# Kernel tuning notes

Hardware: AMD Instinct MI355X
Metric: run time of the kernel (lower is better)

The kernel has to match this reference:

```python
import jax, jax.numpy as jnp
import numpy as np
from math import factorial, comb

N_NODES = 50000
N_EDGES = 640000
FEAT = 32
NUM_BASIS = 8
CUTOFF = 5.0
MAX_Z = 118
NUM_ITERS = 3
LMAX = 2
K = (LMAX + 1) ** 2  # 9 spherical channels for max_degree=2


def _assoc_legendre(c, s, lmax):
    # associated Legendre P_l^m without Condon-Shortley phase
    P = {(0, 0): np.ones_like(c)}
    for m in range(1, lmax + 1):
        P[(m, m)] = P[(m - 1, m - 1)] * (2 * m - 1) * s
    for m in range(lmax):
        P[(m + 1, m)] = (2 * m + 1) * c * P[(m, m)]
    for m in range(lmax + 1):
        for l in range(m + 2, lmax + 1):
            P[(l, m)] = ((2 * l - 1) * c * P[(l - 1, m)] - (l + m - 1) * P[(l - 2, m)]) / (l - m)
    return P


def _real_sh_np(xyz, lmax):
    # Racah-normalized real spherical harmonics (Y_00 = 1), order m=-l..l
    r = np.linalg.norm(xyz, axis=1)
    cth = xyz[:, 2] / r
    sth = np.sqrt(np.maximum(1.0 - cth ** 2, 0.0))
    phi = np.arctan2(xyz[:, 1], xyz[:, 0])
    P = _assoc_legendre(cth, sth, lmax)
    cols = []
    for l in range(lmax + 1):
        for m in range(-l, l + 1):
            am = abs(m)
            if m == 0:
                cols.append(P[(l, 0)])
            else:
                nrm = np.sqrt(2.0 * factorial(l - am) / factorial(l + am))
                ang = np.cos(am * phi) if m > 0 else np.sin(am * phi)
                cols.append(nrm * P[(l, am)] * ang)
    return np.stack(cols, axis=1)


def _gaunt_tensor():
    # cg[k1,k2,k3]: expansion of Y_k1 * Y_k2 onto Y_k3 (degrees <= 2).
    # Products of degree<=2 harmonics lie exactly in span of degree<=4 harmonics,
    # so the least-squares fit below recovers exact coefficients.
    rng = np.random.default_rng(0)
    pts = rng.normal(size=(4096, 3))
    pts /= np.linalg.norm(pts, axis=1, keepdims=True)
    A = _real_sh_np(pts, 2 * LMAX)  # (M, 25)
    Y = A[:, :K]                    # (M, 9)
    prod = (Y[:, :, None] * Y[:, None, :]).reshape(len(pts), K * K)
    coef, *_ = np.linalg.lstsq(A, prod, rcond=None)  # (25, 81)
    return coef[:K].reshape(K, K, K).transpose(1, 2, 0).astype(np.float32)


CG = jnp.asarray(_gaunt_tensor())  # (9, 9, 9)
LOG_BINOM = jnp.asarray([np.log(comb(NUM_BASIS - 1, kk)) for kk in range(NUM_BASIS)], dtype=jnp.float32)


def _sh_l2(u):
    # Racah real SH of unit vectors, degrees 0..2, order m=-l..l
    x, y, z = u[:, 0], u[:, 1], u[:, 2]
    s3 = 1.7320508075688772
    return jnp.stack([
        jnp.ones_like(x),
        y, z, x,
        s3 * x * y, s3 * y * z, 0.5 * (3.0 * z * z - 1.0), s3 * x * z, 0.5 * s3 * (x * x - y * y),
    ], axis=1)


def _radial(r):
    # reciprocal Bernstein basis (log-space, stable) * smooth cutoff
    u = r / (1.0 + r)
    k = jnp.arange(NUM_BASIS, dtype=jnp.float32)
    n = float(NUM_BASIS - 1)
    eps = 1e-12
    logu = jnp.log(jnp.maximum(u, eps))[:, None]
    log1u = jnp.log(jnp.maximum(1.0 - u, eps))[:, None]
    bern = jnp.exp(LOG_BINOM + k * logu + (n - k) * log1u)  # (E, B)
    cut = jnp.where(r < CUTOFF, jnp.exp(-(r * r) / jnp.maximum(CUTOFF * CUTOFF - r * r, eps)), 0.0)
    return bern * cut[:, None]


def _forward(dr_vec, embed, rad_w, d1w, d1b, d2w, d2b, Z, neighbor_idxs):
    idx_i, idx_j = neighbor_idxs[0], neighbor_idxs[1]
    r = jnp.linalg.norm(dr_vec, axis=1)
    u = dr_vec / jnp.maximum(r, 1e-9)[:, None]
    Ysh = _sh_l2(u)              # (E, 9) angular basis
    rad = _radial(r)             # (E, B) radial basis
    # mask padding edges (idx_i == idx_j) as in mask_by_neighbor
    rad = rad * (idx_i != idx_j).astype(rad.dtype)[:, None]

    N = Z.shape[0]
    x = jnp.zeros((N, K, FEAT), jnp.float32).at[:, 0, :].set(embed[Z])

    for i in range(NUM_ITERS):
        last = i == NUM_ITERS - 1
        k3 = 1 if last else K    # last MessagePass has max_degree=0
        xe = x[idx_j]                                  # (E, 9, F) edge gather
        g = jnp.einsum('eb,dbf->edf', rad, rad_w[i])   # (E, 3, F) radial->feature per basis degree
        y = jnp.zeros((N_EDGES, k3, FEAT), jnp.float32)
        for l2 in range(LMAX + 1):
            sl = slice(l2 * l2, (l2 + 1) ** 2)
            c = jnp.einsum('abc,eb->eac', CG[:, sl, :k3], Ysh[:, sl])          # (E, 9, k3)
            y = y + jnp.einsum('eac,eaf->ecf', c, xe * g[:, l2][:, None, :])   # (E, k3, F)
        m = jax.ops.segment_sum(y, idx_i, num_segments=N)                      # scatter-sum
        if last:
            x = x[:, :1, :]      # change_max_degree_or_type(x, 0)
        h = x + m
        h = jnp.einsum('nkf,fg->nkg', h, d1w[i]).at[:, 0, :].add(d1b[i])
        gate = jax.nn.sigmoid(h[:, :1, :])
        h = h * gate             # silu on scalar channel, sigmoid-gated tensor channels
        h = jnp.einsum('nkf,fg->nkg', h, d2w[i]).at[:, 0, :].add(d2b[i])
        x = x + h
    return x[:, 0, :]            # (N, F)


def setup_inputs() -> dict:
    key = jax.random.key(0)
    ks = jax.random.split(key, 8)
    dr_vec = jax.random.normal(ks[0], (N_EDGES, 3), jnp.float32) * 2.0
    Z = jax.random.randint(ks[1], (N_NODES,), 0, MAX_Z + 1, jnp.int32)
    neighbor_idxs = jax.random.randint(ks[2], (2, N_EDGES), 0, N_NODES, jnp.int32)
    embed = jax.random.normal(ks[3], (MAX_Z + 1, FEAT), jnp.float32)
    rad_w = jax.random.normal(ks[4], (NUM_ITERS, LMAX + 1, NUM_BASIS, FEAT), jnp.float32) * 0.5
    d1w = jax.random.normal(ks[5], (NUM_ITERS, FEAT, FEAT), jnp.float32) * (1.0 / np.sqrt(FEAT))
    d1b = jnp.zeros((NUM_ITERS, FEAT), jnp.float32)
    d2w = jax.random.normal(ks[6], (NUM_ITERS, FEAT, FEAT), jnp.float32) * 0.02
    d2b = jnp.zeros((NUM_ITERS, FEAT), jnp.float32)
    return {"dr_vec": dr_vec, "embed": embed, "rad_w": rad_w, "d1w": d1w, "d1b": d1b,
            "d2w": d2w, "d2b": d2b, "Z": Z, "neighbor_idxs": neighbor_idxs}


def reference(dr_vec, embed, rad_w, d1w, d1b, d2w, d2b, Z, neighbor_idxs):
    return _forward(dr_vec, embed, rad_w, d1w, d1b, d2w, d2b, Z, neighbor_idxs)
```

## Files before the change

kernel.cpp:

```cpp
#include <hip/hip_runtime.h>
#include <hip/hip_fp16.h>
#include <math.h>

#define NN 50000
#define NE 640000
#define F  32
#define KCH 9
#define CUT 5.0f

#define C13 (1.0f/3.0f)
#define C23 (2.0f/3.0f)
#define C15 0.2f
#define C25 0.4f
#define C17 (1.0f/7.0f)
#define C27 (2.0f/7.0f)
#define IS3 0.5773502691896258f
#define S35 0.3464101615137755f
#define S37 0.2474358296526968f
#define S3  1.7320508075688772f

#define XH_NODE_B 768

union U2H { unsigned int u; __half2 h; };

__device__ __forceinline__ unsigned int pack2(float a, float b) {
    U2H c; c.h = __floats2half2_rn(a, b); return c.u;
}
__device__ __forceinline__ float2 unpack2(unsigned int u) {
    U2H c; c.u = u; return __half22float2(c.h);
}

__global__ __launch_bounds__(256) void init_x(const float* __restrict__ embed,
                                              const int* __restrict__ Z,
                                              float* __restrict__ x,
                                              char* __restrict__ xh) {
    int idx = blockIdx.x * 256 + threadIdx.x;
    int n = idx >> 5, f = idx & 31;
    float v = embed[Z[n] * F + f];
    float* xp = x + (size_t)n * KCH * F + f;
    xp[0] = v;
    #pragma unroll
    for (int a = 1; a < KCH; ++a) xp[a * F] = 0.f;
    char* bp = xh + (size_t)n * XH_NODE_B + f * 24;
    uint2 u0; u0.x = pack2(v, 0.f); u0.y = 0u;
    uint2 zz; zz.x = 0u; zz.y = 0u;
    *(uint2*)bp = u0;
    *(uint2*)(bp + 8) = zz;
    *(uint2*)(bp + 16) = zz;
}

__global__ __launch_bounds__(256) void hist_kernel(const int* __restrict__ idx_i,
                                                   const int* __restrict__ idx_j,
                                                   const float* __restrict__ dr,
                                                   int* __restrict__ cnt) {
    int e = blockIdx.x * 256 + threadIdx.x;
    if (e >= NE) return;
    int ni = idx_i[e], nj = idx_j[e];
    float dx = dr[3 * e + 0], dy = dr[3 * e + 1], dz = dr[3 * e + 2];
    float r2 = fmaf(dx, dx, fmaf(dy, dy, dz * dz));
    if (ni != nj && r2 < CUT * CUT) atomicAdd(&cnt[ni], 1);
}

#define SCAN_T 1024
#define SCAN_C ((NN + SCAN_T - 1) / SCAN_T)

__global__ __launch_bounds__(SCAN_T) void scan_kernel(const int* __restrict__ cnt,
                                                      int* __restrict__ offs,
                                                      int* __restrict__ head) {
    __shared__ int ps[SCAN_T];
    int t = threadIdx.x;
    int b = t * SCAN_C;
    int e = min(b + SCAN_C, NN);
    int s = 0;
    for (int i = b; i < e; ++i) s += cnt[i];
    ps[t] = s;
    __syncthreads();
    for (int off = 1; off < SCAN_T; off <<= 1) {
        int v = (t >= off) ? ps[t - off] : 0;
        __syncthreads();
        ps[t] += v;
        __syncthreads();
    }
    int run = (t == 0) ? 0 : ps[t - 1];
    for (int i = b; i < e; ++i) { int c = cnt[i]; offs[i] = run; head[i] = run; run += c; }
    if (t == SCAN_T - 1) offs[NN] = ps[SCAN_T - 1];
}

__global__ __launch_bounds__(256) void fill_kernel(const int* __restrict__ idx_i,
                                                   const int* __restrict__ idx_j,
                                                   const float* __restrict__ dr,
                                                   int* __restrict__ head,
                                                   float4* __restrict__ geo) {
    int e = blockIdx.x * 256 + threadIdx.x;
    if (e >= NE) return;
    int ni = idx_i[e], nj = idx_j[e];
    float dx = dr[3 * e + 0], dy = dr[3 * e + 1], dz = dr[3 * e + 2];
    float r2 = fmaf(dx, dx, fmaf(dy, dy, dz * dz));
    if (!(ni != nj && r2 < CUT * CUT)) return;

    float r = sqrtf(r2);
    float inv = 1.0f / fmaxf(r, 1e-9f);
    float ux = dx * inv, uy = dy * inv, uz = dz * inv;

    float cut = expf(-r2 / fmaxf(CUT * CUT - r2, 1e-12f));
    float ur = r / (1.0f + r), vr = 1.0f - ur;
    float up2 = ur*ur, up3 = up2*ur, up4 = up3*ur, up5 = up4*ur, up6 = up5*ur, up7 = up6*ur;
    float vp2 = vr*vr, vp3 = vp2*vr, vp4 = vp3*vr, vp5 = vp4*vr, vp6 = vp5*vr, vp7 = vp6*vr;

    int p = atomicAdd(&head[ni], 1);
    float4 gA, gB, gC;
    gA.x = ux; gA.y = uy; gA.z = uz; gA.w = __int_as_float(nj);
    gB.x = cut * vp7;
    gB.y = cut * 7.f  * ur  * vp6;
    gB.z = cut * 21.f * up2 * vp5;
    gB.w = cut * 35.f * up3 * vp4;
    gC.x = cut * 35.f * up4 * vp3;
    gC.y = cut * 21.f * up5 * vp2;
    gC.z = cut * 7.f  * up6 * vr;
    gC.w = cut * up7;
    geo[(size_t)3 * p + 0] = gA;
    geo[(size_t)3 * p + 1] = gB;
    geo[(size_t)3 * p + 2] = gC;
}

template<int LAST>
__global__ __launch_bounds__(256) void gather_kernel(const float4* __restrict__ geo,
                                                     const char* __restrict__ xh,
                                                     const float* __restrict__ rw_iter,
                                                     const int* __restrict__ offs,
                                                     float* __restrict__ m) {
    const int NWAVES = 2048 * 4;
    int lane = threadIdx.x & 63;
    int wid  = threadIdx.x >> 6;
    int half = lane >> 5;
    int f    = lane & 31;
    int gw   = blockIdx.x * 4 + wid;

    float rwv[24];
    #pragma unroll
    for (int lb = 0; lb < 24; ++lb) rwv[lb] = rw_iter[lb * F + f];
    if (LAST) {
        #pragma unroll
        for (int lb = 8; lb < 16; ++lb) rwv[lb] *= C13;
        #pragma unroll
        for (int lb = 16; lb < 24; ++lb) rwv[lb] *= C15;
    }

    constexpr int NACC = LAST ? 1 : KCH;

    for (int n = gw; n < NN; n += NWAVES) {
        int start = offs[n], end = offs[n + 1];

        float acc[NACC];
        #pragma unroll
        for (int a = 0; a < NACC; ++a) acc[a] = 0.f;

        int t = start + half;
        float4 gA_c = {}, gB_c = {}, gC_c = {}, gA_n = {};
        uint2 xa = {}, xb = {};
        unsigned int xc = 0;

        if (t < end) {
            gA_c = geo[(size_t)3 * t + 0];
            gB_c = geo[(size_t)3 * t + 1];
            gC_c = geo[(size_t)3 * t + 2];
            int njc = __float_as_int(gA_c.w);
            const char* bp = xh + (size_t)njc * XH_NODE_B + f * 24;
            xa = *(const uint2*)bp;
            xb = *(const uint2*)(bp + 8);
            xc = *(const unsigned int*)(bp + 16);
            int t2 = (t + 2 < end) ? t + 2 : t;
            gA_n = geo[(size_t)3 * t2 + 0];
        }

        while (t < end) {
            int tn = t + 2;
            int tnc = (tn < end) ? tn : t;
            int tfc = (tn + 2 < end) ? tn + 2 : tnc;

            float4 gA_f = geo[(size_t)3 * tfc + 0];
            float4 gB_n = geo[(size_t)3 * tnc + 1];
            float4 gC_n = geo[(size_t)3 * tnc + 2];
            int njn = __float_as_int(gA_n.w);
            const char* bp = xh + (size_t)njn * XH_NODE_B + f * 24;
            uint2 na = *(const uint2*)bp;
            uint2 nb = *(const uint2*)(bp + 8);
            unsigned int nc = *(const unsigned int*)(bp + 16);

            float xe[9];
            {
                float2 p;
                p = unpack2(xa.x); xe[0] = p.x; xe[1] = p.y;
                p = unpack2(xa.y); xe[2] = p.x; xe[3] = p.y;
                p = unpack2(xb.x); xe[4] = p.x; xe[5] = p.y;
                p = unpack2(xb.y); xe[6] = p.x; xe[7] = p.y;
                p = unpack2(xc);   xe[8] = p.x;
            }

            float ux = gA_c.x, uy = gA_c.y, uz = gA_c.z;
            float g0, g1, g2;
            g0 = gB_c.x * rwv[0];
            g0 = fmaf(gB_c.y, rwv[1], g0); g0 = fmaf(gB_c.z, rwv[2], g0); g0 = fmaf(gB_c.w, rwv[3], g0);
            g0 = fmaf(gC_c.x, rwv[4], g0); g0 = fmaf(gC_c.y, rwv[5], g0); g0 = fmaf(gC_c.z, rwv[6], g0);
            g0 = fmaf(gC_c.w, rwv[7], g0);
            g1 = gB_c.x * rwv[8];
            g1 = fmaf(gB_c.y, rwv[9],  g1); g1 = fmaf(gB_c.z, rwv[10], g1); g1 = fmaf(gB_c.w, rwv[11], g1);
            g1 = fmaf(gC_c.x, rwv[12], g1); g1 = fmaf(gC_c.y, rwv[13], g1); g1 = fmaf(gC_c.z, rwv[14], g1);
            g1 = fmaf(gC_c.w, rwv[15], g1);
            g2 = gB_c.x * rwv[16];
            g2 = fmaf(gB_c.y, rwv[17], g2); g2 = fmaf(gB_c.z, rwv[18], g2); g2 = fmaf(gB_c.w, rwv[19], g2);
            g2 = fmaf(gC_c.x, rwv[20], g2); g2 = fmaf(gC_c.y, rwv[21], g2); g2 = fmaf(gC_c.z, rwv[22], g2);
            g2 = fmaf(gC_c.w, rwv[23], g2);

            if (LAST) {
                float dot1 = uy * xe[1];
                dot1 = fmaf(uz, xe[2], dot1);
                dot1 = fmaf(ux, xe[3], dot1);
                float Y4 = S3 * ux * uy, Y5 = S3 * uy * uz, Y7 = S3 * ux * uz;
                float Y6 = fmaf(1.5f * uz, uz, -0.5f);
                float Y8 = 0.5f * S3 * (ux * ux - uy * uy);
                float dot2 = Y4 * xe[4];
                dot2 = fmaf(Y5, xe[5], dot2);
                dot2 = fmaf(Y6, xe[6], dot2);
                dot2 = fmaf(Y7, xe[7], dot2);
                dot2 = fmaf(Y8, xe[8], dot2);
                acc[0] = fmaf(g0, xe[0], acc[0]);
                acc[0] = fmaf(g1, dot1, acc[0]);
                acc[0] = fmaf(g2, dot2, acc[0]);
            } else {
                float s2 = S3 * g2;
                float w[9];
                w[0] = g0;
                w[1] = uy * g1; w[2] = uz * g1; w[3] = ux * g1;
                w[4] = s2 * ux * uy;
                w[5] = s2 * uy * uz;
                w[6] = fmaf(1.5f * uz, uz, -0.5f) * g2;
                w[7] = s2 * ux * uz;
                w[8] = 0.5f * s2 * (ux * ux - uy * uy);

                float d0 = xe[0]*w[0], d1 = xe[1]*w[1], d2 = xe[2]*w[2], d3 = xe[3]*w[3];
                float d4 = xe[4]*w[4], d5 = xe[5]*w[5], d6 = xe[6]*w[6], d7 = xe[7]*w[7];
                float d8 = xe[8]*w[8];

                acc[0] += d0 + C13 * (d1 + d2 + d3) + C15 * (d4 + d5 + d6 + d7 + d8);
                #define T(a, b) (xe[a] * w[b] + xe[b] * w[a])
                acc[1] += T(0,1) - C15 * T(1,6) - S35 * T(1,8) + S35 * T(2,5) + S35 * T(3,4);
                acc[2] += T(0,2) + S35 * T(1,5) + C25 * T(2,6) + S35 * T(3,7);
                acc[3] += T(0,3) + S35 * T(1,4) + S35 * T(2,7) - C15 * T(3,6) + S35 * T(3,8);
                acc[4] += T(0,4) + IS3 * T(1,3) - C27 * T(4,6) + S37 * T(5,7);
                acc[5] += T(0,5) + IS3 * T(1,2) + S37 * T(4,7) + C17 * T(5,6) - S37 * T(5,8);
                acc[6] += T(0,6) - C13 * d1 + C23 * d2 - C13 * d3
                        - C27 * d4 + C17 * d5 + C27 * d6 + C17 * d7 - C27 * d8;
                acc[7] += T(0,7) + IS3 * T(2,3) + S37 * T(4,5) + C17 * T(6,7) + S37 * T(7,8);
                acc[8] += T(0,8) - IS3 * d1 + IS3 * d3 - S37 * d5 + S37 * d7 - C27 * T(6,8);
                #undef T
            }

            gA_c = gA_n; gA_n = gA_f;
            gB_c = gB_n; gC_c = gC_n;
            xa = na; xb = nb; xc = nc;
            t = tn;
        }

        #pragma unroll
        for (int a = 0; a < NACC; ++a) acc[a] += __shfl_xor(acc[a], 32);

        if (half == 0) {
            if (LAST) {
                m[(size_t)n * F + f] = acc[0];
            } else {
                float* mp = m + (size_t)n * KCH * F + f;
                #pragma unroll
                for (int a = 0; a < KCH; ++a) mp[a * F] = acc[a];
            }
        }
    }
}

__global__ __launch_bounds__(256) void node_full(float* __restrict__ x,
                                                 const float* __restrict__ m,
                                                 char* __restrict__ xh,
                                                 const float* __restrict__ w1,
                                                 const float* __restrict__ b1,
                                                 const float* __restrict__ w2,
                                                 const float* __restrict__ b2) {
    __shared__ float tile[8][KCH][F];
    int nl = threadIdx.x >> 5, f = threadIdx.x & 31;
    int n = blockIdx.x * 8 + nl;

    float w1c[F];
    #pragma unroll
    for (int fi = 0; fi < F; ++fi) w1c[fi] = w1[fi * F + f];

    float xk[KCH];
    #pragma unroll
    for (int k = 0; k < KCH; ++k) {
        xk[k] = x[((size_t)n * KCH + k) * F + f];
        tile[nl][k][f] = xk[k] + m[((size_t)n * KCH + k) * F + f];
    }
    __syncthreads();

    float o1[KCH];
    #pragma unroll
    for (int k = 0; k < KCH; ++k) {
        float s = 0.f;
        #pragma unroll
        for (int fi = 0; fi < F; ++fi) s = fmaf(tile[nl][k][fi], w1c[fi], s);
        o1[k] = s;
    }
    o1[0] += b1[f];
    float gate = 1.0f / (1.0f + expf(-o1[0]));
    __syncthreads();
    #pragma unroll
    for (int k = 0; k < KCH; ++k) tile[nl][k][f] = o1[k] * gate;
    __syncthreads();

    float w2c[F];
    #pragma unroll
    for (int fi = 0; fi < F; ++fi) w2c[fi] = w2[fi * F + f];

    float xn[KCH];
    #pragma unroll
    for (int k = 0; k < KCH; ++k) {
        float s = (k == 0) ? b2[f] : 0.f;
        #pragma unroll
        for (int fi = 0; fi < F; ++fi) s = fmaf(tile[nl][k][fi], w2c[fi], s);
        xn[k] = xk[k] + s;
        x[((size_t)n * KCH + k) * F + f] = xn[k];
    }

    char* bp = xh + (size_t)n * XH_NODE_B + f * 24;
    uint2 u0, u1, u2;
    u0.x = pack2(xn[0], xn[1]); u0.y = pack2(xn[2], xn[3]);
    u1.x = pack2(xn[4], xn[5]); u1.y = pack2(xn[6], xn[7]);
    u2.x = pack2(xn[8], 0.f);   u2.y = 0u;
    *(uint2*)bp = u0;
    *(uint2*)(bp + 8) = u1;
    *(uint2*)(bp + 16) = u2;
}

__global__ __launch_bounds__(256) void node_last(const float* __restrict__ x,
                                                 const float* __restrict__ m1,
                                                 const float* __restrict__ w1,
                                                 const float* __restrict__ b1,
                                                 const float* __restrict__ w2,
                                                 const float* __restrict__ b2,
                                                 float* __restrict__ out) {
    __shared__ float tile[8][F];
    int nl = threadIdx.x >> 5, f = threadIdx.x & 31;
    int n = blockIdx.x * 8 + nl;

    float w1c[F];
    #pragma unroll
    for (int fi = 0; fi < F; ++fi) w1c[fi] = w1[fi * F + f];

    float x0 = x[(size_t)n * KCH * F + f];
    tile[nl][f] = x0 + m1[(size_t)n * F + f];
    __syncthreads();
    float s = 0.f;
    #pragma unroll
    for (int fi = 0; fi < F; ++fi) s = fmaf(tile[nl][fi], w1c[fi], s);
    s += b1[f];
    float gate = 1.0f / (1.0f + expf(-s));
    float h2 = s * gate;
    __syncthreads();
    tile[nl][f] = h2;
    __syncthreads();
    float w2c[F];
    #pragma unroll
    for (int fi = 0; fi < F; ++fi) w2c[fi] = w2[fi * F + f];
    float o = b2[f];
    #pragma unroll
    for (int fi = 0; fi < F; ++fi) o = fmaf(tile[nl][fi], w2c[fi], o);
    out[(size_t)n * F + f] = x0 + o;
}

extern "C" void kernel_launch(void* const* d_in, const int* in_sizes, int n_in,
                              void* d_out, int out_size, void* d_ws, size_t ws_size,
                              hipStream_t stream) {
    (void)in_sizes; (void)n_in; (void)out_size; (void)ws_size;
    const float* dr    = (const float*)d_in[0];
    const float* embed = (const float*)d_in[1];
    const float* rad_w = (const float*)d_in[2];
    const float* d1w   = (const float*)d_in[3];
    const float* d1b   = (const float*)d_in[4];
    const float* d2w   = (const float*)d_in[5];
    const float* d2b   = (const float*)d_in[6];
    const int*   Z     = (const int*)d_in[7];
    const int*   nidx  = (const int*)d_in[8];
    const int* idx_i = nidx;
    const int* idx_j = nidx + NE;

    float* x = (float*)d_ws;
    float* m = x + (size_t)NN * KCH * F;
    char*  xh = (char*)(m + (size_t)NN * KCH * F);
    float4* geo = (float4*)(xh + (size_t)NN * XH_NODE_B);
    int* offs = (int*)(geo + (size_t)3 * (NE + 1));
    int* head = offs + (NN + 1);
    int* cnt  = head + NN;
    float* outp = (float*)d_out;

    hipMemsetAsync(cnt, 0, NN * sizeof(int), stream);
    hist_kernel<<<(NE + 255) / 256, 256, 0, stream>>>(idx_i, idx_j, dr, cnt);
    scan_kernel<<<1, SCAN_T, 0, stream>>>(cnt, offs, head);
    fill_kernel<<<(NE + 255) / 256, 256, 0, stream>>>(idx_i, idx_j, dr, head, geo);

    init_x<<<NN * F / 256, 256, 0, stream>>>(embed, Z, x, xh);

    for (int i = 0; i < 3; ++i) {
        const float* rwi = rad_w + (size_t)i * 3 * 8 * F;
        const float* w1 = d1w + (size_t)i * F * F;
        const float* b1 = d1b + (size_t)i * F;
        const float* w2 = d2w + (size_t)i * F * F;
        const float* b2 = d2b + (size_t)i * F;
        if (i < 2) {
            gather_kernel<0><<<2048, 256, 0, stream>>>(geo, xh, rwi, offs, m);
            node_full<<<NN / 8, 256, 0, stream>>>(x, m, xh, w1, b1, w2, b2);
        } else {
            gather_kernel<1><<<2048, 256, 0, stream>>>(geo, xh, rwi, offs, m);
            node_last<<<NN / 8, 256, 0, stream>>>(x, m, w1, b1, w2, b2, outp);
        }
    }
}
```

Measured before the change: 699.4 us.

## Pack per-edge geometry into fp16 records with separate neighbor index array

Edge geometry (unit vector and eight radial basis values) is now stored as fp16 pairs in three uint2 words per edge instead of three float4s, with the neighbor index moved to its own int array. This halves the per-edge record traffic the gather kernel reads on each of its three passes and lets the index prefetch run independently of the geometry loads. The gather kernel also gets a launch-bounds occupancy hint. In exchange, the unit vectors and radial coefficients lose precision to fp16.

```diff
diff --git a/kernel.cpp b/kernel.cpp
--- a/kernel.cpp
+++ b/kernel.cpp
@@ -90,7 +90,8 @@
                                                    const int* __restrict__ idx_j,
                                                    const float* __restrict__ dr,
                                                    int* __restrict__ head,
-                                                   float4* __restrict__ geo) {
+                                                   uint2* __restrict__ erec,
+                                                   int* __restrict__ njarr) {
     int e = blockIdx.x * 256 + threadIdx.x;
     if (e >= NE) return;
     int ni = idx_i[e], nj = idx_j[e];
@@ -107,28 +108,33 @@
     float up2 = ur*ur, up3 = up2*ur, up4 = up3*ur, up5 = up4*ur, up6 = up5*ur, up7 = up6*ur;
     float vp2 = vr*vr, vp3 = vp2*vr, vp4 = vp3*vr, vp5 = vp4*vr, vp6 = vp5*vr, vp7 = vp6*vr;
 
+    float rc0 = cut * vp7;
+    float rc1 = cut * 7.f  * ur  * vp6;
+    float rc2 = cut * 21.f * up2 * vp5;
+    float rc3 = cut * 35.f * up3 * vp4;
+    float rc4 = cut * 35.f * up4 * vp3;
+    float rc5 = cut * 21.f * up5 * vp2;
+    float rc6 = cut * 7.f  * up6 * vr;
+    float rc7 = cut * up7;
+
     int p = atomicAdd(&head[ni], 1);
-    float4 gA, gB, gC;
-    gA.x = ux; gA.y = uy; gA.z = uz; gA.w = __int_as_float(nj);
-    gB.x = cut * vp7;
-    gB.y = cut * 7.f  * ur  * vp6;
-    gB.z = cut * 21.f * up2 * vp5;
-    gB.w = cut * 35.f * up3 * vp4;
-    gC.x = cut * 35.f * up4 * vp3;
-    gC.y = cut * 21.f * up5 * vp2;
-    gC.z = cut * 7.f  * up6 * vr;
-    gC.w = cut * up7;
-    geo[(size_t)3 * p + 0] = gA;
-    geo[(size_t)3 * p + 1] = gB;
-    geo[(size_t)3 * p + 2] = gC;
+    uint2 e0, e1, e2;
+    e0.x = pack2(ux, uy); e0.y = pack2(uz, 0.f);
+    e1.x = pack2(rc0, rc1); e1.y = pack2(rc2, rc3);
+    e2.x = pack2(rc4, rc5); e2.y = pack2(rc6, rc7);
+    erec[(size_t)3 * p + 0] = e0;
+    erec[(size_t)3 * p + 1] = e1;
+    erec[(size_t)3 * p + 2] = e2;
+    njarr[p] = nj;
 }
 
 template<int LAST>
-__global__ __launch_bounds__(256) void gather_kernel(const float4* __restrict__ geo,
-                                                     const char* __restrict__ xh,
-                                                     const float* __restrict__ rw_iter,
-                                                     const int* __restrict__ offs,
-                                                     float* __restrict__ m) {
+__global__ __launch_bounds__(256, 8) void gather_kernel(const uint2* __restrict__ erec,
+                                                        const int* __restrict__ njarr,
+                                                        const char* __restrict__ xh,
+                                                        const float* __restrict__ rw_iter,
+                                                        const int* __restrict__ offs,
+                                                        float* __restrict__ m) {
     const int NWAVES = 2048 * 4;
     int lane = threadIdx.x & 63;
     int wid  = threadIdx.x >> 6;
@@ -156,21 +162,22 @@
         for (int a = 0; a < NACC; ++a) acc[a] = 0.f;
 
         int t = start + half;
-        float4 gA_c = {}, gB_c = {}, gC_c = {}, gA_n = {};
-        uint2 xa = {}, xb = {};
-        unsigned int xc = 0;
+        uint2 e0_c = {}, e1_c = {}, e2_c = {};
+        uint2 xa_c = {}, xb_c = {};
+        unsigned int xc_c = 0;
+        int nj_n = 0;
 
         if (t < end) {
-            gA_c = geo[(size_t)3 * t + 0];
-            gB_c = geo[(size_t)3 * t + 1];
-            gC_c = geo[(size_t)3 * t + 2];
-            int njc = __float_as_int(gA_c.w);
-            const char* bp = xh + (size_t)njc * XH_NODE_B + f * 24;
-            xa = *(const uint2*)bp;
-            xb = *(const uint2*)(bp + 8);
-            xc = *(const unsigned int*)(bp + 16);
+            e0_c = erec[(size_t)3 * t + 0];
+            e1_c = erec[(size_t)3 * t + 1];
+            e2_c = erec[(size_t)3 * t + 2];
+            int nj0 = njarr[t];
+            const char* bp = xh + (size_t)nj0 * XH_NODE_B + f * 24;
+            xa_c = *(const uint2*)bp;
+            xb_c = *(const uint2*)(bp + 8);
+            xc_c = *(const unsigned int*)(bp + 16);
             int t2 = (t + 2 < end) ? t + 2 : t;
-            gA_n = geo[(size_t)3 * t2 + 0];
+            nj_n = njarr[t2];
         }
 
         while (t < end) {
@@ -178,39 +185,46 @@
             int tnc = (tn < end) ? tn : t;
             int tfc = (tn + 2 < end) ? tn + 2 : tnc;
 
-            float4 gA_f = geo[(size_t)3 * tfc + 0];
-            float4 gB_n = geo[(size_t)3 * tnc + 1];
-            float4 gC_n = geo[(size_t)3 * tnc + 2];
-            int njn = __float_as_int(gA_n.w);
-            const char* bp = xh + (size_t)njn * XH_NODE_B + f * 24;
-            uint2 na = *(const uint2*)bp;
-            uint2 nb = *(const uint2*)(bp + 8);
-            unsigned int nc = *(const unsigned int*)(bp + 16);
+            uint2 e0_n = erec[(size_t)3 * tnc + 0];
+            uint2 e1_n = erec[(size_t)3 * tnc + 1];
+            uint2 e2_n = erec[(size_t)3 * tnc + 2];
+            int nj_f = njarr[tfc];
+            const char* bp = xh + (size_t)nj_n * XH_NODE_B + f * 24;
+            uint2 xa_n = *(const uint2*)bp;
+            uint2 xb_n = *(const uint2*)(bp + 8);
+            unsigned int xc_n = *(const unsigned int*)(bp + 16);
+
+            float2 uxy = unpack2(e0_c.x);
+            float ux = uxy.x, uy = uxy.y;
+            float uz = unpack2(e0_c.y).x;
+            float2 rcA = unpack2(e1_c.x);
+            float2 rcB = unpack2(e1_c.y);
+            float2 rcC = unpack2(e2_c.x);
+            float2 rcD = unpack2(e2_c.y);
 
             float xe[9];
             {
                 float2 p;
-                p = unpack2(xa.x); xe[0] = p.x; xe[1] = p.y;
-                p = unpack2(xa.y); xe[2] = p.x; xe[3] = p.y;
-                p = unpack2(xb.x); xe[4] = p.x; xe[5] = p.y;
-                p = unpack2(xb.y); xe[6] = p.x; xe[7] = p.y;
-                p = unpack2(xc);   xe[8] = p.x;
+                p = unpack2(xa_c.x); xe[0] = p.x; xe[1] = p.y;
+                p = unpack2(xa_c.y); xe[2] = p.x; xe[3] = p.y;
+                p = unpack2(xb_c.x); xe[4] = p.x; xe[5] = p.y;
+                p = unpack2(xb_c.y); xe[6] = p.x; xe[7] = p.y;
+                p = unpack2(xc_c);   xe[8] = p.x;
             }
 
-            float ux = gA_c.x, uy = gA_c.y, uz = gA_c.z;
             float g0, g1, g2;
-            g0 = gB_c.x * rwv[0];
-            g0 = fmaf(gB_c.y, rwv[1], g0); g0 = fmaf(gB_c.z, rwv[2], g0); g0 = fmaf(gB_c.w, rwv[3], g0);
-            g0 = fmaf(gC_c.x, rwv[4], g0); g0 = fmaf(gC_c.y, rwv[5], g0); g0 = fmaf(gC_c.z, rwv[6], g0);
-            g0 = fmaf(gC_c.w, rwv[7], g0);
-            g1 = gB_c.x * rwv[8];
-            g1 = fmaf(gB_c.y, rwv[9],  g1); g1 = fmaf(gB_c.z, rwv[10], g1); g1 = fmaf(gB_c.w, rwv[11], g1);
-            g1 = fmaf(gC_c.x, rwv[12], g1); g1 = fmaf(gC_c.y, rwv[13], g1); g1 = fmaf(gC_c.z, rwv[14], g1);
-            g1 = fmaf(gC_c.w, rwv[15], g1);
-            g2 = gB_c.x * rwv[16];
-            g2 = fmaf(gB_c.y, rwv[17], g2); g2 = fmaf(gB_c.z, rwv[18], g2); g2 = fmaf(gB_c.w, rwv[19], g2);
-            g2 = fmaf(gC_c.x, rwv[20], g2); g2 = fmaf(gC_c.y, rwv[21], g2); g2 = fmaf(gC_c.z, rwv[22], g2);
-            g2 = fmaf(gC_c.w, rwv[23], g2);
+            g0 = rcA.x * rwv[0];
+            g0 = fmaf(rcA.y, rwv[1], g0); g0 = fmaf(rcB.x, rwv[2], g0); g0 = fmaf(rcB.y, rwv[3], g0);
+            g0 = fmaf(rcC.x, rwv[4], g0); g0 = fmaf(rcC.y, rwv[5], g0); g0 = fmaf(rcD.x, rwv[6], g0);
+            g0 = fmaf(rcD.y, rwv[7], g0);
+            g1 = rcA.x * rwv[8];
+            g1 = fmaf(rcA.y, rwv[9],  g1); g1 = fmaf(rcB.x, rwv[10], g1); g1 = fmaf(rcB.y, rwv[11], g1);
+            g1 = fmaf(rcC.x, rwv[12], g1); g1 = fmaf(rcC.y, rwv[13], g1); g1 = fmaf(rcD.x, rwv[14], g1);
+            g1 = fmaf(rcD.y, rwv[15], g1);
+            g2 = rcA.x * rwv[16];
+            g2 = fmaf(rcA.y, rwv[17], g2); g2 = fmaf(rcB.x, rwv[18], g2); g2 = fmaf(rcB.y, rwv[19], g2);
+            g2 = fmaf(rcC.x, rwv[20], g2); g2 = fmaf(rcC.y, rwv[21], g2); g2 = fmaf(rcD.x, rwv[22], g2);
+            g2 = fmaf(rcD.y, rwv[23], g2);
 
             if (LAST) {
                 float dot1 = uy * xe[1];
@@ -256,9 +270,9 @@
                 #undef T
             }
 
-            gA_c = gA_n; gA_n = gA_f;
-            gB_c = gB_n; gC_c = gC_n;
-            xa = na; xb = nb; xc = nc;
+            e0_c = e0_n; e1_c = e1_n; e2_c = e2_n;
+            xa_c = xa_n; xb_c = xb_n; xc_c = xc_n;
+            nj_n = nj_f;
             t = tn;
         }
 
@@ -394,8 +408,9 @@
     float* x = (float*)d_ws;
     float* m = x + (size_t)NN * KCH * F;
     char*  xh = (char*)(m + (size_t)NN * KCH * F);
-    float4* geo = (float4*)(xh + (size_t)NN * XH_NODE_B);
-    int* offs = (int*)(geo + (size_t)3 * (NE + 1));
+    uint2* erec = (uint2*)(xh + (size_t)NN * XH_NODE_B);
+    int* njarr = (int*)(erec + (size_t)3 * NE);
+    int* offs = njarr + NE;
     int* head = offs + (NN + 1);
     int* cnt  = head + NN;
     float* outp = (float*)d_out;
@@ -403,7 +418,7 @@
     hipMemsetAsync(cnt, 0, NN * sizeof(int), stream);
     hist_kernel<<<(NE + 255) / 256, 256, 0, stream>>>(idx_i, idx_j, dr, cnt);
     scan_kernel<<<1, SCAN_T, 0, stream>>>(cnt, offs, head);
-    fill_kernel<<<(NE + 255) / 256, 256, 0, stream>>>(idx_i, idx_j, dr, head, geo);
+    fill_kernel<<<(NE + 255) / 256, 256, 0, stream>>>(idx_i, idx_j, dr, head, erec, njarr);
 
     init_x<<<NN * F / 256, 256, 0, stream>>>(embed, Z, x, xh);
 
@@ -414,10 +429,10 @@
         const float* w2 = d2w + (size_t)i * F * F;
         const float* b2 = d2b + (size_t)i * F;
         if (i < 2) {
-            gather_kernel<0><<<2048, 256, 0, stream>>>(geo, xh, rwi, offs, m);
+            gather_kernel<0><<<2048, 256, 0, stream>>>(erec, njarr, xh, rwi, offs, m);
             node_full<<<NN / 8, 256, 0, stream>>>(x, m, xh, w1, b1, w2, b2);
         } else {
-            gather_kernel<1><<<2048, 256, 0, stream>>>(geo, xh, rwi, offs, m);
+            gather_kernel<1><<<2048, 256, 0, stream>>>(erec, njarr, xh, rwi, offs, m);
             node_last<<<NN / 8, 256, 0, stream>>>(x, m, w1, b1, w2, b2, outp);
         }
     }
```

Result: slower. 2.255 ms (+222.5%).
